# Kernel optimization log

Measured on AMD Instinct MI355X. Metric: run time of the kernel, lower is better.

Reference implementation:

```python
import jax, jax.numpy as jnp
import numpy as np

ATTEN_DIM = 64

def setup_inputs() -> dict:
    key = jax.random.key(0)
    ks = jax.random.split(key, 7)
    b, c, h, w = 16, 2048, 32, 32
    d_att, d_emb = 64, 64
    x = jax.random.normal(ks[0], (b, c, h, w), dtype=jnp.float32)
    # 1x1 conv == per-position linear; store weights as [out, in]
    scale = 1.0 / np.sqrt(c)
    wq = jax.random.normal(ks[1], (d_att, c), dtype=jnp.float32) * scale
    wk = jax.random.normal(ks[2], (d_att, c), dtype=jnp.float32) * scale
    wv = jax.random.normal(ks[3], (d_emb, c), dtype=jnp.float32) * scale
    bq = jnp.zeros((d_att,), dtype=jnp.float32)
    bk = jnp.zeros((d_att,), dtype=jnp.float32)
    bv = jnp.zeros((d_emb,), dtype=jnp.float32)
    return {"x": x, "wq": wq, "bq": bq, "wk": wk, "bk": bk, "wv": wv, "bv": bv}


def reference(x, wq, bq, wk, bk, wv, bv):
    b, c, h, w = x.shape
    # 1x1 conv projections: [b,c,h,w] x [d,c] -> [b,d,h,w]
    q = jnp.einsum('bchw,dc->bdhw', x, wq) + bq[None, :, None, None]
    k = jnp.einsum('bchw,dc->bdhw', x, wk) + bk[None, :, None, None]
    v = jnp.einsum('bchw,dc->bdhw', x, wv) + bv[None, :, None, None]
    # full non-local attention scores [b, h, w, h, w]
    atten = jnp.einsum('bcxy,bcij->bxyij', q, k) / ATTEN_DIM  # NOTE: module divides by atten_dim, not sqrt
    atten = jax.nn.softmax(atten.reshape(b, h, w, h * w), axis=-1).reshape(b, h, w, h, w)
    out = jnp.einsum('bxyij,bdij->bxyd', atten, v)
    return jnp.transpose(out, (0, 3, 1, 2))  # [b, emb_dim, h, w]
```

## Files before the change

kernel.cpp:

```cpp
#include <hip/hip_runtime.h>

typedef float f32x4 __attribute__((ext_vector_type(4)));
typedef short s16x8 __attribute__((ext_vector_type(8)));
typedef unsigned short u16;
typedef unsigned short u16x8 __attribute__((ext_vector_type(8)));

__device__ __forceinline__ u16 f2bf(float f) {
  unsigned u = __builtin_bit_cast(unsigned, f);
  u += 0x7fffu + ((u >> 16) & 1u);
  return (u16)(u >> 16);
}

__device__ __forceinline__ unsigned cvt_pk_bf16(float a, float b) {
  unsigned r;
  asm("v_cvt_pk_bf16_f32 %0, %1, %2" : "=v"(r) : "v"(a), "v"(b));
  return r;
}

#define AS1 __attribute__((address_space(1)))
#define AS3 __attribute__((address_space(3)))
#define GLD16(g, l) __builtin_amdgcn_global_load_lds((const AS1 unsigned int*)(g), (AS3 unsigned int*)(l), 16, 0, 0)

#define CEXP 0.0225421101f

__global__ __launch_bounds__(256) void prepack_w(
    const float* __restrict__ wq, const float* __restrict__ wk, const float* __restrict__ wv,
    u16* __restrict__ Wpk)
{
  const int d = blockIdx.x;
  const int t = threadIdx.x;
  const int kc = t >> 3, blk = t & 7;
  const int key = (d >> 1) & 7;
  const float* src = (d < 64) ? (wq + (size_t)d * 2048)
                   : (d < 128) ? (wk + (size_t)(d - 64) * 2048)
                               : (wv + (size_t)(d - 128) * 2048);
  const float* s8 = src + kc * 64 + ((blk ^ key) << 3);
  u16x8 o;
#pragma unroll
  for (int j = 0; j < 8; ++j) o[j] = f2bf(s8[j]);
  *(u16x8*)(Wpk + ((size_t)(kc * 192 + d) << 6) + (blk << 3)) = o;
}

__global__ __launch_bounds__(512) void qkv_proj(
    const float* __restrict__ x, const u16* __restrict__ Wpk,
    const float* __restrict__ bq, const float* __restrict__ bk, const float* __restrict__ bv,
    u16* __restrict__ Qo, u16* __restrict__ Ko, u16* __restrict__ Vt)
{
  const int b   = blockIdx.x >> 4;
  const int p0  = (blockIdx.x & 15) * 64;
  const int tid = threadIdx.x;
  const int lane = tid & 63;
  const int wid  = tid >> 6;
  const int l15 = lane & 15, l4 = lane >> 4;
  const int wm = wid & 1, wn = wid >> 1;

  __shared__ __align__(16) u16 lA[4][64 * 64];
  __shared__ __align__(16) u16 lB[4][192 * 64];

  const int pg = lane & 15;
  const int kb = wid * 4 + (lane >> 4);
  const int k0 = kb * 4;
  const int ww = wid - 4;

  f32x4 acc[2][3];
#pragma unroll
  for (int m = 0; m < 2; ++m)
#pragma unroll
    for (int n = 0; n < 3; ++n) acc[m][n] = (f32x4)(0.0f);

  const float* xb = x + (size_t)b * 2048 * 1024 + p0 + pg * 4;
  float4 SA[8], SB[8];

  auto xload2 = [&](int c, float4 (&S)[8]) {
#pragma unroll
    for (int cc = 0; cc < 2; ++cc) {
      const float* g = xb + (size_t)((c + cc) * 64 + k0) * 1024;
#pragma unroll
      for (int r = 0; r < 4; ++r) S[cc * 4 + r] = *(const float4*)(g + r * 1024);
    }
  };
  auto xstore2 = [&](int c, float4 (&S)[8]) {
#pragma unroll
    for (int cc = 0; cc < 2; ++cc) {
      const int slot = (c + cc) & 3;
#pragma unroll
      for (int col = 0; col < 4; ++col) {
        int p = pg * 4 + col;
        unsigned lo = cvt_pk_bf16(S[cc * 4 + 0][col], S[cc * 4 + 1][col]);
        unsigned hi = cvt_pk_bf16(S[cc * 4 + 2][col], S[cc * 4 + 3][col]);
        int swz = ((kb >> 1) ^ ((p >> 1) & 7)) & 7;
        char* dst = (char*)&lA[0][0] + slot * 8192 + p * 128 + (swz << 4) + (kb & 1) * 8;
        *(uint2*)dst = make_uint2(lo, hi);
      }
    }
  };
  auto wissue2 = [&](int c) {
#pragma unroll
    for (int cc = 0; cc < 2; ++cc) {
      const int slot = (c + cc) & 3;
      const u16* g = Wpk + (size_t)(c + cc) * 12288 + lane * 8;
#pragma unroll
      for (int j = 0; j < 6; ++j) {
        int q = ww * 6 + j;
        GLD16(g + q * 512, &lB[0][0] + slot * 12288 + q * 512);
      }
    }
  };
  auto domfma = [&](int slot) {
#pragma unroll
    for (int ks = 0; ks < 2; ++ks) {
      s16x8 af[2], bfv[3];
#pragma unroll
      for (int m = 0; m < 2; ++m) {
        int p = wm * 32 + m * 16 + l15;
        int swz = ((ks * 4 + l4) ^ ((p >> 1) & 7)) & 7;
        af[m] = *(const s16x8*)((const char*)&lA[0][0] + slot * 8192 + p * 128 + (swz << 4));
      }
#pragma unroll
      for (int n = 0; n < 3; ++n) {
        int d = wn * 48 + n * 16 + l15;
        int swz = ((ks * 4 + l4) ^ ((d >> 1) & 7)) & 7;
        bfv[n] = *(const s16x8*)((const char*)&lB[0][0] + slot * 24576 + d * 128 + (swz << 4));
      }
#pragma unroll
      for (int m = 0; m < 2; ++m)
#pragma unroll
        for (int n = 0; n < 3; ++n)
          acc[m][n] = __builtin_amdgcn_mfma_f32_16x16x32_bf16(af[m], bfv[n], acc[m][n], 0, 0, 0);
    }
  };
  auto barrier = [&]() {
    if (wid < 4) asm volatile("s_waitcnt lgkmcnt(0)" ::: "memory");
    else         asm volatile("s_waitcnt vmcnt(0) lgkmcnt(0)" ::: "memory");
    __builtin_amdgcn_sched_barrier(0);
    __builtin_amdgcn_s_barrier();
    __builtin_amdgcn_sched_barrier(0);
  };
  auto step = [&](int t, float4 (&Sl)[8], float4 (&Ss)[8]) {
    if (wid < 4) { if (t < 14) xload2(2 * t + 4, Sl); }
    else         { if (t < 15) wissue2(2 * t + 2); }
    __builtin_amdgcn_s_setprio(1);
    domfma((2 * t) & 3);
    domfma((2 * t + 1) & 3);
    __builtin_amdgcn_s_setprio(0);
    if (wid < 4 && t < 15) xstore2(2 * t + 2, Ss);
    barrier();
  };

  if (wid < 4) { xload2(0, SA); xload2(2, SB); xstore2(0, SA); }
  else         { wissue2(0); }
  barrier();

  for (int tt = 0; tt < 8; ++tt) {
    step(2 * tt,     SA, SB);
    step(2 * tt + 1, SB, SA);
  }

#pragma unroll
  for (int n = 0; n < 3; ++n) {
    const int dg = wn * 48 + n * 16 + l15;
    const int wi = dg >> 6, dl = dg & 63;
    const float* bsrc = (wi == 0) ? bq : (wi == 1) ? bk : bv;
    const float bias = bsrc[dl];
#pragma unroll
    for (int m = 0; m < 2; ++m) {
      const int pl = wm * 32 + m * 16 + l4 * 4;
      f32x4 a = acc[m][n];
      if (wi == 0) {
        u16* dst = Qo + ((size_t)b * 1024 + p0 + pl) * 64 + dl;
#pragma unroll
        for (int r = 0; r < 4; ++r) dst[(size_t)r * 64] = f2bf((a[r] + bias) * CEXP);
      } else if (wi == 1) {
#pragma unroll
        for (int r = 0; r < 4; ++r) {
          const int p = p0 + pl + r;
          Ko[((size_t)b * 1024 + p) * 64 + (((dl >> 3) ^ ((p >> 1) & 7)) << 3) + (dl & 7)]
            = f2bf(a[r] + bias);
        }
      } else {
        const int pk0 = p0 + pl;
        ushort4 hh;
        hh.x = f2bf(a[0] + bias); hh.y = f2bf(a[1] + bias);
        hh.z = f2bf(a[2] + bias); hh.w = f2bf(a[3] + bias);
        u16* dst = Vt + ((size_t)b * 64 + dl) * 1024 + (pk0 & ~127)
                 + (((((pk0 >> 3) & 15) ^ ((dl & 7) << 1)) & 15) << 3) + (pk0 & 7);
        *(ushort4*)dst = hh;
      }
    }
  }
}

__global__ __launch_bounds__(256) void attn_kernel(
    const u16* __restrict__ Qg, const u16* __restrict__ Kg,
    const u16* __restrict__ Vg, float* __restrict__ Po, float* __restrict__ lp)
{
  const int bid = blockIdx.x;
  const int b  = bid >> 5;
  const int qt = (bid >> 1) & 15;
  const int h  = bid & 1;
  const int q0 = qt * 64;
  const int tid = threadIdx.x;
  const int lane = tid & 63;
  const int w = tid >> 6;
  const int l15 = lane & 15, l4 = lane >> 4;
  const int qb = q0 + w * 16;

  __shared__ __align__(16) u16 lK[2][128 * 64];
  __shared__ __align__(16) u16 lV[2][64 * 128];
  __shared__ __align__(16) u16 lP[4][16 * 128];

  s16x8 qa[2];
#pragma unroll
  for (int ks = 0; ks < 2; ++ks)
    qa[ks] = *(const s16x8*)(Qg + ((size_t)b * 1024 + qb + l15) * 64 + ks * 32 + l4 * 8);

  const u16* Kb = Kg + (size_t)b * 65536;
  const u16* Vb = Vg + (size_t)b * 65536;

  float l_run[4];
  f32x4 oacc[4];
#pragma unroll
  for (int r = 0; r < 4; ++r) l_run[r] = 0.f;
#pragma unroll
  for (int n = 0; n < 4; ++n) oacc[n] = (f32x4)(0.0f);

  auto kv_issue = [&](int tile, int buf) {
    const int pk0 = tile * 128;
#pragma unroll
    for (int jj = 0; jj < 4; ++jj)
      GLD16(Kb + (size_t)(pk0 + w * 32 + jj * 8) * 64 + lane * 8,
            (char*)&lK[buf][0] + (w * 4 + jj) * 1024);
#pragma unroll
    for (int jj = 0; jj < 4; ++jj)
      GLD16(Vb + (size_t)(w * 16 + jj * 4 + (lane >> 4)) * 1024 + pk0 + (lane & 15) * 8,
            (char*)&lV[buf][0] + (w * 4 + jj) * 1024);
  };

  auto compute = [&](int buf) {
    f32x4 sacc[8];
#pragma unroll
    for (int n = 0; n < 8; ++n) sacc[n] = (f32x4)(0.0f);
    __builtin_amdgcn_s_setprio(1);
#pragma unroll
    for (int ks = 0; ks < 2; ++ks) {
#pragma unroll
      for (int n = 0; n < 8; ++n) {
        int row = n * 16 + l15;
        s16x8 kv = *(const s16x8*)(&lK[buf][0] + row * 64 +
                     (((ks * 4 + l4) ^ ((row >> 1) & 7)) << 3));
        sacc[n] = __builtin_amdgcn_mfma_f32_16x16x32_bf16(qa[ks], kv, sacc[n], 0, 0, 0);
      }
    }
    __builtin_amdgcn_s_setprio(0);

#pragma unroll
    for (int r = 0; r < 4; ++r) {
      const int prow = l4 * 4 + r;
      const int key = (prow & 7) << 1;
      float pv[8];
      float psum = 0.f;
#pragma unroll
      for (int n = 0; n < 8; ++n) { pv[n] = exp2f(sacc[n][r]); psum += pv[n]; }
#pragma unroll
      for (int n = 0; n < 8; n += 2) {
        unsigned pk = cvt_pk_bf16(pv[n], pv[n + 1]);
        int blk0 = (n * 2 + (l15 >> 3)) ^ key;
        int blk1 = ((n + 1) * 2 + (l15 >> 3)) ^ key;
        lP[w][prow * 128 + blk0 * 8 + (l15 & 7)] = (u16)pk;
        lP[w][prow * 128 + blk1 * 8 + (l15 & 7)] = (u16)(pk >> 16);
      }
      psum += __shfl_xor(psum, 1);
      psum += __shfl_xor(psum, 2);
      psum += __shfl_xor(psum, 4);
      psum += __shfl_xor(psum, 8);
      l_run[r] += psum;
    }

    __builtin_amdgcn_s_setprio(1);
#pragma unroll
    for (int ks = 0; ks < 4; ++ks) {
      s16x8 pfr = *(const s16x8*)(&lP[w][0] + l15 * 128 +
                    (((ks * 4 + l4) ^ ((l15 & 7) << 1)) << 3));
#pragma unroll
      for (int n = 0; n < 4; ++n) {
        int row = n * 16 + l15;
        s16x8 vv = *(const s16x8*)(&lV[buf][0] + row * 128 +
                     (((ks * 4 + l4) ^ ((row & 7) << 1)) << 3));
        oacc[n] = __builtin_amdgcn_mfma_f32_16x16x32_bf16(pfr, vv, oacc[n], 0, 0, 0);
      }
    }
    __builtin_amdgcn_s_setprio(0);
  };

  const int t0 = h * 4;
  kv_issue(t0, 0);
  kv_issue(t0 + 1, 1);
  asm volatile("s_waitcnt vmcnt(8)" ::: "memory");
  __builtin_amdgcn_sched_barrier(0);
  __builtin_amdgcn_s_barrier();
  __builtin_amdgcn_sched_barrier(0);

  for (int ic = 0; ic < 4; ++ic) {
    compute(ic & 1);
    if (ic < 3) {
      __builtin_amdgcn_sched_barrier(0);
      __builtin_amdgcn_s_barrier();
      __builtin_amdgcn_sched_barrier(0);
      if (ic + 2 < 4) {
        kv_issue(t0 + ic + 2, ic & 1);
        asm volatile("s_waitcnt vmcnt(8)" ::: "memory");
      } else {
        asm volatile("s_waitcnt vmcnt(0)" ::: "memory");
      }
      __builtin_amdgcn_sched_barrier(0);
      __builtin_amdgcn_s_barrier();
      __builtin_amdgcn_sched_barrier(0);
    }
  }

#pragma unroll
  for (int n = 0; n < 4; ++n) {
    const int d = n * 16 + l15;
    float4 o;
    o.x = oacc[n][0]; o.y = oacc[n][1]; o.z = oacc[n][2]; o.w = oacc[n][3];
    *(float4*)(Po + (((size_t)h * 16 + b) * 64 + d) * 1024 + q0 + w * 16 + l4 * 4) = o;
  }
  if (l15 == 0) {
#pragma unroll
    for (int r = 0; r < 4; ++r)
      lp[((size_t)h * 16 + b) * 1024 + qb + l4 * 4 + r] = l_run[r];
  }
}

__global__ __launch_bounds__(256) void attn_merge(
    const float* __restrict__ Po, const float* __restrict__ lp, float* __restrict__ out)
{
  const int i = (blockIdx.x * 256 + threadIdx.x) * 4;
  float4 a = *(const float4*)(Po + i);
  float4 c = *(const float4*)(Po + 1048576 + i);
  const int b = i >> 16;
  const int p = i & 1023;
  const float* l0 = lp + b * 1024 + p;
  const float* l1 = lp + 16384 + b * 1024 + p;
  float4 o;
  o.x = (a.x + c.x) / (l0[0] + l1[0]);
  o.y = (a.y + c.y) / (l0[1] + l1[1]);
  o.z = (a.z + c.z) / (l0[2] + l1[2]);
  o.w = (a.w + c.w) / (l0[3] + l1[3]);
  *(float4*)(out + i) = o;
}

extern "C" void kernel_launch(void* const* d_in, const int* in_sizes, int n_in,
                              void* d_out, int out_size, void* d_ws, size_t ws_size,
                              hipStream_t stream) {
  const float* x  = (const float*)d_in[0];
  const float* wq = (const float*)d_in[1];
  const float* bq = (const float*)d_in[2];
  const float* wk = (const float*)d_in[3];
  const float* bk = (const float*)d_in[4];
  const float* wv = (const float*)d_in[5];
  const float* bv = (const float*)d_in[6];
  float* out = (float*)d_out;

  u16* Qo  = (u16*)d_ws;
  u16* Ko  = Qo + (size_t)16 * 1024 * 64;
  u16* Vt  = Ko + (size_t)16 * 1024 * 64;
  u16* Wpk = Vt + (size_t)16 * 1024 * 64;
  float* Po = (float*)(Wpk + (size_t)32 * 192 * 64);
  float* lpart = Po + (size_t)2 * 16 * 64 * 1024;

  prepack_w<<<192, 256, 0, stream>>>(wq, wk, wv, Wpk);
  qkv_proj<<<256, 512, 0, stream>>>(x, Wpk, bq, bk, bv, Qo, Ko, Vt);
  attn_kernel<<<512, 256, 0, stream>>>(Qo, Ko, Vt, Po, lpart);
  attn_merge<<<1024, 256, 0, stream>>>(Po, lpart, out);
}
```

Before: 57.26 us.

## Fuse all four kernels into one cooperative persistent kernel with grid syncs

Replaces the prepack, QKV projection, attention and merge launches with one cooperative kernel of 256 blocks by 512 threads, separated by grid.sync barriers. The two key-halves of attention now run as two 256-thread halves of the same block and are merged through shared memory, which removes the global partial-output buffer and the separate merge pass. This is meant to cut launch gaps and global round-trips. In exchange it adds two grid-wide barriers and halves the attention grid to 256 blocks with a large 160KB shared allocation, so occupancy and parallelism drop.

```diff
diff --git a/kernel.cpp b/kernel.cpp
--- a/kernel.cpp
+++ b/kernel.cpp
@@ -1,4 +1,7 @@
 #include <hip/hip_runtime.h>
+#include <hip/hip_cooperative_groups.h>
+
+namespace cg = cooperative_groups;
 
 typedef float f32x4 __attribute__((ext_vector_type(4)));
 typedef short s16x8 __attribute__((ext_vector_type(8)));
@@ -23,331 +26,327 @@
 
 #define CEXP 0.0225421101f
 
-__global__ __launch_bounds__(256) void prepack_w(
-    const float* __restrict__ wq, const float* __restrict__ wk, const float* __restrict__ wv,
+__global__ __launch_bounds__(512) void fused_all(
+    const float* __restrict__ x,
+    const float* __restrict__ wq, const float* __restrict__ bq,
+    const float* __restrict__ wk, const float* __restrict__ bk,
+    const float* __restrict__ wv, const float* __restrict__ bv,
+    float* __restrict__ out,
+    u16* __restrict__ Qo, u16* __restrict__ Ko, u16* __restrict__ Vt,
     u16* __restrict__ Wpk)
 {
-  const int d = blockIdx.x;
-  const int t = threadIdx.x;
-  const int kc = t >> 3, blk = t & 7;
-  const int key = (d >> 1) & 7;
-  const float* src = (d < 64) ? (wq + (size_t)d * 2048)
-                   : (d < 128) ? (wk + (size_t)(d - 64) * 2048)
-                               : (wv + (size_t)(d - 128) * 2048);
-  const float* s8 = src + kc * 64 + ((blk ^ key) << 3);
-  u16x8 o;
-#pragma unroll
-  for (int j = 0; j < 8; ++j) o[j] = f2bf(s8[j]);
-  *(u16x8*)(Wpk + ((size_t)(kc * 192 + d) << 6) + (blk << 3)) = o;
-}
-
-__global__ __launch_bounds__(512) void qkv_proj(
-    const float* __restrict__ x, const u16* __restrict__ Wpk,
-    const float* __restrict__ bq, const float* __restrict__ bk, const float* __restrict__ bv,
-    u16* __restrict__ Qo, u16* __restrict__ Ko, u16* __restrict__ Vt)
-{
-  const int b   = blockIdx.x >> 4;
-  const int p0  = (blockIdx.x & 15) * 64;
+  cg::grid_group grid = cg::this_grid();
+  const int bid = blockIdx.x;
   const int tid = threadIdx.x;
   const int lane = tid & 63;
   const int wid  = tid >> 6;
   const int l15 = lane & 15, l4 = lane >> 4;
-  const int wm = wid & 1, wn = wid >> 1;
-
-  __shared__ __align__(16) u16 lA[4][64 * 64];
-  __shared__ __align__(16) u16 lB[4][192 * 64];
-
-  const int pg = lane & 15;
-  const int kb = wid * 4 + (lane >> 4);
-  const int k0 = kb * 4;
-  const int ww = wid - 4;
-
-  f32x4 acc[2][3];
-#pragma unroll
-  for (int m = 0; m < 2; ++m)
-#pragma unroll
-    for (int n = 0; n < 3; ++n) acc[m][n] = (f32x4)(0.0f);
-
-  const float* xb = x + (size_t)b * 2048 * 1024 + p0 + pg * 4;
-  float4 SA[8], SB[8];
-
-  auto xload2 = [&](int c, float4 (&S)[8]) {
-#pragma unroll
-    for (int cc = 0; cc < 2; ++cc) {
-      const float* g = xb + (size_t)((c + cc) * 64 + k0) * 1024;
-#pragma unroll
-      for (int r = 0; r < 4; ++r) S[cc * 4 + r] = *(const float4*)(g + r * 1024);
-    }
-  };
-  auto xstore2 = [&](int c, float4 (&S)[8]) {
-#pragma unroll
-    for (int cc = 0; cc < 2; ++cc) {
-      const int slot = (c + cc) & 3;
-#pragma unroll
-      for (int col = 0; col < 4; ++col) {
-        int p = pg * 4 + col;
-        unsigned lo = cvt_pk_bf16(S[cc * 4 + 0][col], S[cc * 4 + 1][col]);
-        unsigned hi = cvt_pk_bf16(S[cc * 4 + 2][col], S[cc * 4 + 3][col]);
-        int swz = ((kb >> 1) ^ ((p >> 1) & 7)) & 7;
-        char* dst = (char*)&lA[0][0] + slot * 8192 + p * 128 + (swz << 4) + (kb & 1) * 8;
-        *(uint2*)dst = make_uint2(lo, hi);
-      }
-    }
-  };
-  auto wissue2 = [&](int c) {
-#pragma unroll
-    for (int cc = 0; cc < 2; ++cc) {
-      const int slot = (c + cc) & 3;
-      const u16* g = Wpk + (size_t)(c + cc) * 12288 + lane * 8;
-#pragma unroll
-      for (int j = 0; j < 6; ++j) {
-        int q = ww * 6 + j;
-        GLD16(g + q * 512, &lB[0][0] + slot * 12288 + q * 512);
-      }
-    }
-  };
-  auto domfma = [&](int slot) {
-#pragma unroll
-    for (int ks = 0; ks < 2; ++ks) {
-      s16x8 af[2], bfv[3];
+  const int b  = bid >> 4;
+  const int p0 = (bid & 15) * 64;
+
+  __shared__ __align__(16) char smem[163840];
+
+  if (tid < 192) {
+    const int Gv = bid * 192 + tid;
+    const int kc = Gv / 1536;
+    const int r  = Gv % 1536;
+    const int d  = r >> 3;
+    const int blk = r & 7;
+    const int key = (d >> 1) & 7;
+    const float* src = (d < 64) ? (wq + (size_t)d * 2048)
+                     : (d < 128) ? (wk + (size_t)(d - 64) * 2048)
+                                 : (wv + (size_t)(d - 128) * 2048);
+    const float* s8 = src + kc * 64 + ((blk ^ key) << 3);
+    u16x8 o;
+#pragma unroll
+    for (int j = 0; j < 8; ++j) o[j] = f2bf(s8[j]);
+    *(u16x8*)(Wpk + ((size_t)(kc * 192 + d) << 6) + (blk << 3)) = o;
+  }
+  __threadfence();
+  grid.sync();
+
+  {
+    const int wm = wid & 1, wn = wid >> 1;
+    const int pg = lane & 15;
+    const int kb = wid * 4 + (lane >> 4);
+    const int k0 = kb * 4;
+    const int ww = wid - 4;
+
+    f32x4 acc[2][3];
+#pragma unroll
+    for (int m = 0; m < 2; ++m)
+#pragma unroll
+      for (int n = 0; n < 3; ++n) acc[m][n] = (f32x4)(0.0f);
+
+    const float* xb = x + (size_t)b * 2048 * 1024 + p0 + pg * 4;
+    float4 SA[8], SB[8];
+
+    auto xload2 = [&](int c, float4 (&S)[8]) {
+#pragma unroll
+      for (int cc = 0; cc < 2; ++cc) {
+        const float* g = xb + (size_t)((c + cc) * 64 + k0) * 1024;
+#pragma unroll
+        for (int r = 0; r < 4; ++r) S[cc * 4 + r] = *(const float4*)(g + r * 1024);
+      }
+    };
+    auto xstore2 = [&](int c, float4 (&S)[8]) {
+#pragma unroll
+      for (int cc = 0; cc < 2; ++cc) {
+        const int slot = (c + cc) & 3;
+#pragma unroll
+        for (int col = 0; col < 4; ++col) {
+          int p = pg * 4 + col;
+          unsigned lo = cvt_pk_bf16(S[cc * 4 + 0][col], S[cc * 4 + 1][col]);
+          unsigned hi = cvt_pk_bf16(S[cc * 4 + 2][col], S[cc * 4 + 3][col]);
+          int swz = ((kb >> 1) ^ ((p >> 1) & 7)) & 7;
+          *(uint2*)(smem + slot * 8192 + p * 128 + (swz << 4) + (kb & 1) * 8)
+            = make_uint2(lo, hi);
+        }
+      }
+    };
+    auto wissue2 = [&](int c) {
+#pragma unroll
+      for (int cc = 0; cc < 2; ++cc) {
+        const int slot = (c + cc) & 3;
+        const u16* g = Wpk + (size_t)(c + cc) * 12288 + lane * 8;
+#pragma unroll
+        for (int j = 0; j < 6; ++j) {
+          int q = ww * 6 + j;
+          GLD16(g + q * 512, smem + 32768 + slot * 24576 + q * 1024);
+        }
+      }
+    };
+    auto domfma = [&](int slot) {
+#pragma unroll
+      for (int ks = 0; ks < 2; ++ks) {
+        s16x8 af[2], bfv[3];
+#pragma unroll
+        for (int m = 0; m < 2; ++m) {
+          int p = wm * 32 + m * 16 + l15;
+          int swz = ((ks * 4 + l4) ^ ((p >> 1) & 7)) & 7;
+          af[m] = *(const s16x8*)(smem + slot * 8192 + p * 128 + (swz << 4));
+        }
+#pragma unroll
+        for (int n = 0; n < 3; ++n) {
+          int d = wn * 48 + n * 16 + l15;
+          int swz = ((ks * 4 + l4) ^ ((d >> 1) & 7)) & 7;
+          bfv[n] = *(const s16x8*)(smem + 32768 + slot * 24576 + d * 128 + (swz << 4));
+        }
+#pragma unroll
+        for (int m = 0; m < 2; ++m)
+#pragma unroll
+          for (int n = 0; n < 3; ++n)
+            acc[m][n] = __builtin_amdgcn_mfma_f32_16x16x32_bf16(af[m], bfv[n], acc[m][n], 0, 0, 0);
+      }
+    };
+    auto barrier = [&]() {
+      if (wid < 4) asm volatile("s_waitcnt lgkmcnt(0)" ::: "memory");
+      else         asm volatile("s_waitcnt vmcnt(0) lgkmcnt(0)" ::: "memory");
+      __builtin_amdgcn_sched_barrier(0);
+      __builtin_amdgcn_s_barrier();
+      __builtin_amdgcn_sched_barrier(0);
+    };
+    auto step = [&](int t, float4 (&Sl)[8], float4 (&Ss)[8]) {
+      if (wid < 4) { if (t < 14) xload2(2 * t + 4, Sl); }
+      else         { if (t < 15) wissue2(2 * t + 2); }
+      __builtin_amdgcn_s_setprio(1);
+      domfma((2 * t) & 3);
+      domfma((2 * t + 1) & 3);
+      __builtin_amdgcn_s_setprio(0);
+      if (wid < 4 && t < 15) xstore2(2 * t + 2, Ss);
+      barrier();
+    };
+
+    if (wid < 4) { xload2(0, SA); xload2(2, SB); xstore2(0, SA); }
+    else         { wissue2(0); }
+    barrier();
+
+    for (int tt = 0; tt < 8; ++tt) {
+      step(2 * tt,     SA, SB);
+      step(2 * tt + 1, SB, SA);
+    }
+
+#pragma unroll
+    for (int n = 0; n < 3; ++n) {
+      const int dg = wn * 48 + n * 16 + l15;
+      const int wi = dg >> 6, dl = dg & 63;
+      const float* bsrc = (wi == 0) ? bq : (wi == 1) ? bk : bv;
+      const float bias = bsrc[dl];
 #pragma unroll
       for (int m = 0; m < 2; ++m) {
-        int p = wm * 32 + m * 16 + l15;
-        int swz = ((ks * 4 + l4) ^ ((p >> 1) & 7)) & 7;
-        af[m] = *(const s16x8*)((const char*)&lA[0][0] + slot * 8192 + p * 128 + (swz << 4));
-      }
-#pragma unroll
-      for (int n = 0; n < 3; ++n) {
-        int d = wn * 48 + n * 16 + l15;
-        int swz = ((ks * 4 + l4) ^ ((d >> 1) & 7)) & 7;
-        bfv[n] = *(const s16x8*)((const char*)&lB[0][0] + slot * 24576 + d * 128 + (swz << 4));
-      }
-#pragma unroll
-      for (int m = 0; m < 2; ++m)
-#pragma unroll
-        for (int n = 0; n < 3; ++n)
-          acc[m][n] = __builtin_amdgcn_mfma_f32_16x16x32_bf16(af[m], bfv[n], acc[m][n], 0, 0, 0);
-    }
-  };
-  auto barrier = [&]() {
-    if (wid < 4) asm volatile("s_waitcnt lgkmcnt(0)" ::: "memory");
-    else         asm volatile("s_waitcnt vmcnt(0) lgkmcnt(0)" ::: "memory");
+        const int pl = wm * 32 + m * 16 + l4 * 4;
+        f32x4 a = acc[m][n];
+        if (wi == 0) {
+          u16* dst = Qo + ((size_t)b * 1024 + p0 + pl) * 64 + dl;
+#pragma unroll
+          for (int r = 0; r < 4; ++r) dst[(size_t)r * 64] = f2bf((a[r] + bias) * CEXP);
+        } else if (wi == 1) {
+#pragma unroll
+          for (int r = 0; r < 4; ++r) {
+            const int p = p0 + pl + r;
+            Ko[((size_t)b * 1024 + p) * 64 + (((dl >> 3) ^ ((p >> 1) & 7)) << 3) + (dl & 7)]
+              = f2bf(a[r] + bias);
+          }
+        } else {
+          const int pk0 = p0 + pl;
+          ushort4 hh;
+          hh.x = f2bf(a[0] + bias); hh.y = f2bf(a[1] + bias);
+          hh.z = f2bf(a[2] + bias); hh.w = f2bf(a[3] + bias);
+          u16* dst = Vt + ((size_t)b * 64 + dl) * 1024 + (pk0 & ~127)
+                   + (((((pk0 >> 3) & 15) ^ ((dl & 7) << 1)) & 15) << 3) + (pk0 & 7);
+          *(ushort4*)dst = hh;
+        }
+      }
+    }
+  }
+  __threadfence();
+  grid.sync();
+
+  {
+    const int h = wid >> 2;
+    const int w = wid & 3;
+    const int q0 = p0;
+    char* gbase = smem + h * 65536;
+    char* lPw   = smem + 131072 + wid * 4096;
+
+    s16x8 qa[2];
+#pragma unroll
+    for (int ks = 0; ks < 2; ++ks)
+      qa[ks] = *(const s16x8*)(Qo + ((size_t)b * 1024 + q0 + w * 16 + l15) * 64
+                               + ks * 32 + l4 * 8);
+
+    const u16* Kb = Ko + (size_t)b * 65536;
+    const u16* Vb = Vt + (size_t)b * 65536;
+
+    float l_run[4];
+    f32x4 oacc[4];
+#pragma unroll
+    for (int r = 0; r < 4; ++r) l_run[r] = 0.f;
+#pragma unroll
+    for (int n = 0; n < 4; ++n) oacc[n] = (f32x4)(0.0f);
+
+    auto kv_issue = [&](int tile, int buf) {
+      const int pk0 = tile * 128;
+#pragma unroll
+      for (int jj = 0; jj < 4; ++jj)
+        GLD16(Kb + (size_t)(pk0 + w * 32 + jj * 8) * 64 + lane * 8,
+              gbase + buf * 16384 + (w * 4 + jj) * 1024);
+#pragma unroll
+      for (int jj = 0; jj < 4; ++jj)
+        GLD16(Vb + (size_t)(w * 16 + jj * 4 + (lane >> 4)) * 1024 + pk0 + (lane & 15) * 8,
+              gbase + 32768 + buf * 16384 + (w * 4 + jj) * 1024);
+    };
+
+    auto compute = [&](int buf) {
+      const char* kB = gbase + buf * 16384;
+      const char* vB = gbase + 32768 + buf * 16384;
+      f32x4 sacc[8];
+#pragma unroll
+      for (int n = 0; n < 8; ++n) sacc[n] = (f32x4)(0.0f);
+      __builtin_amdgcn_s_setprio(1);
+#pragma unroll
+      for (int ks = 0; ks < 2; ++ks) {
+#pragma unroll
+        for (int n = 0; n < 8; ++n) {
+          int row = n * 16 + l15;
+          s16x8 kv = *(const s16x8*)(kB + row * 128 +
+                       ((((ks * 4 + l4) ^ ((row >> 1) & 7)) & 7) << 4));
+          sacc[n] = __builtin_amdgcn_mfma_f32_16x16x32_bf16(qa[ks], kv, sacc[n], 0, 0, 0);
+        }
+      }
+      __builtin_amdgcn_s_setprio(0);
+
+#pragma unroll
+      for (int r = 0; r < 4; ++r) {
+        const int prow = l4 * 4 + r;
+        const int key = (prow & 7) << 1;
+        float pv[8];
+        float psum = 0.f;
+#pragma unroll
+        for (int n = 0; n < 8; ++n) { pv[n] = exp2f(sacc[n][r]); psum += pv[n]; }
+#pragma unroll
+        for (int n = 0; n < 8; n += 2) {
+          unsigned pk = cvt_pk_bf16(pv[n], pv[n + 1]);
+          int blk0 = ((n * 2 + (l15 >> 3)) ^ key) & 15;
+          int blk1 = (((n + 1) * 2 + (l15 >> 3)) ^ key) & 15;
+          *(u16*)(lPw + prow * 256 + blk0 * 16 + (l15 & 7) * 2) = (u16)pk;
+          *(u16*)(lPw + prow * 256 + blk1 * 16 + (l15 & 7) * 2) = (u16)(pk >> 16);
+        }
+        psum += __shfl_xor(psum, 1);
+        psum += __shfl_xor(psum, 2);
+        psum += __shfl_xor(psum, 4);
+        psum += __shfl_xor(psum, 8);
+        l_run[r] += psum;
+      }
+
+      __builtin_amdgcn_s_setprio(1);
+#pragma unroll
+      for (int ks = 0; ks < 4; ++ks) {
+        s16x8 pfr = *(const s16x8*)(lPw + l15 * 256 +
+                      ((((ks * 4 + l4) ^ ((l15 & 7) << 1)) & 15) << 4));
+#pragma unroll
+        for (int n = 0; n < 4; ++n) {
+          int row = n * 16 + l15;
+          s16x8 vv = *(const s16x8*)(vB + row * 256 +
+                       ((((ks * 4 + l4) ^ ((row & 7) << 1)) & 15) << 4));
+          oacc[n] = __builtin_amdgcn_mfma_f32_16x16x32_bf16(pfr, vv, oacc[n], 0, 0, 0);
+        }
+      }
+      __builtin_amdgcn_s_setprio(0);
+    };
+
+    const int t0 = h * 4;
+    kv_issue(t0, 0);
+    kv_issue(t0 + 1, 1);
+    asm volatile("s_waitcnt vmcnt(8)" ::: "memory");
     __builtin_amdgcn_sched_barrier(0);
     __builtin_amdgcn_s_barrier();
     __builtin_amdgcn_sched_barrier(0);
-  };
-  auto step = [&](int t, float4 (&Sl)[8], float4 (&Ss)[8]) {
-    if (wid < 4) { if (t < 14) xload2(2 * t + 4, Sl); }
-    else         { if (t < 15) wissue2(2 * t + 2); }
-    __builtin_amdgcn_s_setprio(1);
-    domfma((2 * t) & 3);
-    domfma((2 * t + 1) & 3);
-    __builtin_amdgcn_s_setprio(0);
-    if (wid < 4 && t < 15) xstore2(2 * t + 2, Ss);
-    barrier();
-  };
-
-  if (wid < 4) { xload2(0, SA); xload2(2, SB); xstore2(0, SA); }
-  else         { wissue2(0); }
-  barrier();
-
-  for (int tt = 0; tt < 8; ++tt) {
-    step(2 * tt,     SA, SB);
-    step(2 * tt + 1, SB, SA);
+
+    for (int ic = 0; ic < 4; ++ic) {
+      compute(ic & 1);
+      if (ic < 3) {
+        __builtin_amdgcn_sched_barrier(0);
+        __builtin_amdgcn_s_barrier();
+        __builtin_amdgcn_sched_barrier(0);
+        if (ic + 2 < 4) {
+          kv_issue(t0 + ic + 2, ic & 1);
+          asm volatile("s_waitcnt vmcnt(8)" ::: "memory");
+        } else {
+          asm volatile("s_waitcnt vmcnt(0)" ::: "memory");
+        }
+        __builtin_amdgcn_sched_barrier(0);
+        __builtin_amdgcn_s_barrier();
+        __builtin_amdgcn_sched_barrier(0);
+      }
+    }
+
+    __syncthreads();
+    if (h == 1) {
+      float* mrg = (float*)smem + (tid - 256) * 20;
+#pragma unroll
+      for (int n = 0; n < 4; ++n) *(f32x4*)(mrg + n * 4) = oacc[n];
+#pragma unroll
+      for (int r = 0; r < 4; ++r) mrg[16 + r] = l_run[r];
+    }
+    __syncthreads();
+    if (h == 0) {
+      const float* mrg = (const float*)smem + tid * 20;
+      float lr[4];
+#pragma unroll
+      for (int r = 0; r < 4; ++r) lr[r] = l_run[r] + mrg[16 + r];
+#pragma unroll
+      for (int n = 0; n < 4; ++n) {
+        f32x4 o1 = *(const f32x4*)(mrg + n * 4);
+        float4 o;
+        o.x = (oacc[n][0] + o1[0]) / lr[0];
+        o.y = (oacc[n][1] + o1[1]) / lr[1];
+        o.z = (oacc[n][2] + o1[2]) / lr[2];
+        o.w = (oacc[n][3] + o1[3]) / lr[3];
+        *(float4*)(out + ((size_t)b * 64 + n * 16 + l15) * 1024 + q0 + w * 16 + l4 * 4) = o;
+      }
+    }
   }
-
-#pragma unroll
-  for (int n = 0; n < 3; ++n) {
-    const int dg = wn * 48 + n * 16 + l15;
-    const int wi = dg >> 6, dl = dg & 63;
-    const float* bsrc = (wi == 0) ? bq : (wi == 1) ? bk : bv;
-    const float bias = bsrc[dl];
-#pragma unroll
-    for (int m = 0; m < 2; ++m) {
-      const int pl = wm * 32 + m * 16 + l4 * 4;
-      f32x4 a = acc[m][n];
-      if (wi == 0) {
-        u16* dst = Qo + ((size_t)b * 1024 + p0 + pl) * 64 + dl;
-#pragma unroll
-        for (int r = 0; r < 4; ++r) dst[(size_t)r * 64] = f2bf((a[r] + bias) * CEXP);
-      } else if (wi == 1) {
-#pragma unroll
-        for (int r = 0; r < 4; ++r) {
-          const int p = p0 + pl + r;
-          Ko[((size_t)b * 1024 + p) * 64 + (((dl >> 3) ^ ((p >> 1) & 7)) << 3) + (dl & 7)]
-            = f2bf(a[r] + bias);
-        }
-      } else {
-        const int pk0 = p0 + pl;
-        ushort4 hh;
-        hh.x = f2bf(a[0] + bias); hh.y = f2bf(a[1] + bias);
-        hh.z = f2bf(a[2] + bias); hh.w = f2bf(a[3] + bias);
-        u16* dst = Vt + ((size_t)b * 64 + dl) * 1024 + (pk0 & ~127)
-                 + (((((pk0 >> 3) & 15) ^ ((dl & 7) << 1)) & 15) << 3) + (pk0 & 7);
-        *(ushort4*)dst = hh;
-      }
-    }
-  }
-}
-
-__global__ __launch_bounds__(256) void attn_kernel(
-    const u16* __restrict__ Qg, const u16* __restrict__ Kg,
-    const u16* __restrict__ Vg, float* __restrict__ Po, float* __restrict__ lp)
-{
-  const int bid = blockIdx.x;
-  const int b  = bid >> 5;
-  const int qt = (bid >> 1) & 15;
-  const int h  = bid & 1;
-  const int q0 = qt * 64;
-  const int tid = threadIdx.x;
-  const int lane = tid & 63;
-  const int w = tid >> 6;
-  const int l15 = lane & 15, l4 = lane >> 4;
-  const int qb = q0 + w * 16;
-
-  __shared__ __align__(16) u16 lK[2][128 * 64];
-  __shared__ __align__(16) u16 lV[2][64 * 128];
-  __shared__ __align__(16) u16 lP[4][16 * 128];
-
-  s16x8 qa[2];
-#pragma unroll
-  for (int ks = 0; ks < 2; ++ks)
-    qa[ks] = *(const s16x8*)(Qg + ((size_t)b * 1024 + qb + l15) * 64 + ks * 32 + l4 * 8);
-
-  const u16* Kb = Kg + (size_t)b * 65536;
-  const u16* Vb = Vg + (size_t)b * 65536;
-
-  float l_run[4];
-  f32x4 oacc[4];
-#pragma unroll
-  for (int r = 0; r < 4; ++r) l_run[r] = 0.f;
-#pragma unroll
-  for (int n = 0; n < 4; ++n) oacc[n] = (f32x4)(0.0f);
-
-  auto kv_issue = [&](int tile, int buf) {
-    const int pk0 = tile * 128;
-#pragma unroll
-    for (int jj = 0; jj < 4; ++jj)
-      GLD16(Kb + (size_t)(pk0 + w * 32 + jj * 8) * 64 + lane * 8,
-            (char*)&lK[buf][0] + (w * 4 + jj) * 1024);
-#pragma unroll
-    for (int jj = 0; jj < 4; ++jj)
-      GLD16(Vb + (size_t)(w * 16 + jj * 4 + (lane >> 4)) * 1024 + pk0 + (lane & 15) * 8,
-            (char*)&lV[buf][0] + (w * 4 + jj) * 1024);
-  };
-
-  auto compute = [&](int buf) {
-    f32x4 sacc[8];
-#pragma unroll
-    for (int n = 0; n < 8; ++n) sacc[n] = (f32x4)(0.0f);
-    __builtin_amdgcn_s_setprio(1);
-#pragma unroll
-    for (int ks = 0; ks < 2; ++ks) {
-#pragma unroll
-      for (int n = 0; n < 8; ++n) {
-        int row = n * 16 + l15;
-        s16x8 kv = *(const s16x8*)(&lK[buf][0] + row * 64 +
-                     (((ks * 4 + l4) ^ ((row >> 1) & 7)) << 3));
-        sacc[n] = __builtin_amdgcn_mfma_f32_16x16x32_bf16(qa[ks], kv, sacc[n], 0, 0, 0);
-      }
-    }
-    __builtin_amdgcn_s_setprio(0);
-
-#pragma unroll
-    for (int r = 0; r < 4; ++r) {
-      const int prow = l4 * 4 + r;
-      const int key = (prow & 7) << 1;
-      float pv[8];
-      float psum = 0.f;
-#pragma unroll
-      for (int n = 0; n < 8; ++n) { pv[n] = exp2f(sacc[n][r]); psum += pv[n]; }
-#pragma unroll
-      for (int n = 0; n < 8; n += 2) {
-        unsigned pk = cvt_pk_bf16(pv[n], pv[n + 1]);
-        int blk0 = (n * 2 + (l15 >> 3)) ^ key;
-        int blk1 = ((n + 1) * 2 + (l15 >> 3)) ^ key;
-        lP[w][prow * 128 + blk0 * 8 + (l15 & 7)] = (u16)pk;
-        lP[w][prow * 128 + blk1 * 8 + (l15 & 7)] = (u16)(pk >> 16);
-      }
-      psum += __shfl_xor(psum, 1);
-      psum += __shfl_xor(psum, 2);
-      psum += __shfl_xor(psum, 4);
-      psum += __shfl_xor(psum, 8);
-      l_run[r] += psum;
-    }
-
-    __builtin_amdgcn_s_setprio(1);
-#pragma unroll
-    for (int ks = 0; ks < 4; ++ks) {
-      s16x8 pfr = *(const s16x8*)(&lP[w][0] + l15 * 128 +
-                    (((ks * 4 + l4) ^ ((l15 & 7) << 1)) << 3));
-#pragma unroll
-      for (int n = 0; n < 4; ++n) {
-        int row = n * 16 + l15;
-        s16x8 vv = *(const s16x8*)(&lV[buf][0] + row * 128 +
-                     (((ks * 4 + l4) ^ ((row & 7) << 1)) << 3));
-        oacc[n] = __builtin_amdgcn_mfma_f32_16x16x32_bf16(pfr, vv, oacc[n], 0, 0, 0);
-      }
-    }
-    __builtin_amdgcn_s_setprio(0);
-  };
-
-  const int t0 = h * 4;
-  kv_issue(t0, 0);
-  kv_issue(t0 + 1, 1);
-  asm volatile("s_waitcnt vmcnt(8)" ::: "memory");
-  __builtin_amdgcn_sched_barrier(0);
-  __builtin_amdgcn_s_barrier();
-  __builtin_amdgcn_sched_barrier(0);
-
-  for (int ic = 0; ic < 4; ++ic) {
-    compute(ic & 1);
-    if (ic < 3) {
-      __builtin_amdgcn_sched_barrier(0);
-      __builtin_amdgcn_s_barrier();
-      __builtin_amdgcn_sched_barrier(0);
-      if (ic + 2 < 4) {
-        kv_issue(t0 + ic + 2, ic & 1);
-        asm volatile("s_waitcnt vmcnt(8)" ::: "memory");
-      } else {
-        asm volatile("s_waitcnt vmcnt(0)" ::: "memory");
-      }
-      __builtin_amdgcn_sched_barrier(0);
-      __builtin_amdgcn_s_barrier();
-      __builtin_amdgcn_sched_barrier(0);
-    }
-  }
-
-#pragma unroll
-  for (int n = 0; n < 4; ++n) {
-    const int d = n * 16 + l15;
-    float4 o;
-    o.x = oacc[n][0]; o.y = oacc[n][1]; o.z = oacc[n][2]; o.w = oacc[n][3];
-    *(float4*)(Po + (((size_t)h * 16 + b) * 64 + d) * 1024 + q0 + w * 16 + l4 * 4) = o;
-  }
-  if (l15 == 0) {
-#pragma unroll
-    for (int r = 0; r < 4; ++r)
-      lp[((size_t)h * 16 + b) * 1024 + qb + l4 * 4 + r] = l_run[r];
-  }
-}
-
-__global__ __launch_bounds__(256) void attn_merge(
-    const float* __restrict__ Po, const float* __restrict__ lp, float* __restrict__ out)
-{
-  const int i = (blockIdx.x * 256 + threadIdx.x) * 4;
-  float4 a = *(const float4*)(Po + i);
-  float4 c = *(const float4*)(Po + 1048576 + i);
-  const int b = i >> 16;
-  const int p = i & 1023;
-  const float* l0 = lp + b * 1024 + p;
-  const float* l1 = lp + 16384 + b * 1024 + p;
-  float4 o;
-  o.x = (a.x + c.x) / (l0[0] + l1[0]);
-  o.y = (a.y + c.y) / (l0[1] + l1[1]);
-  o.z = (a.z + c.z) / (l0[2] + l1[2]);
-  o.w = (a.w + c.w) / (l0[3] + l1[3]);
-  *(float4*)(out + i) = o;
 }
 
 extern "C" void kernel_launch(void* const* d_in, const int* in_sizes, int n_in,
@@ -366,11 +365,9 @@
   u16* Ko  = Qo + (size_t)16 * 1024 * 64;
   u16* Vt  = Ko + (size_t)16 * 1024 * 64;
   u16* Wpk = Vt + (size_t)16 * 1024 * 64;
-  float* Po = (float*)(Wpk + (size_t)32 * 192 * 64);
-  float* lpart = Po + (size_t)2 * 16 * 64 * 1024;
-
-  prepack_w<<<192, 256, 0, stream>>>(wq, wk, wv, Wpk);
-  qkv_proj<<<256, 512, 0, stream>>>(x, Wpk, bq, bk, bv, Qo, Ko, Vt);
-  attn_kernel<<<512, 256, 0, stream>>>(Qo, Ko, Vt, Po, lpart);
-  attn_merge<<<1024, 256, 0, stream>>>(Po, lpart, out);
+
+  void* args[] = { (void*)&x, (void*)&wq, (void*)&bq, (void*)&wk, (void*)&bk,
+                   (void*)&wv, (void*)&bv, (void*)&out,
+                   (void*)&Qo, (void*)&Ko, (void*)&Vt, (void*)&Wpk };
+  hipLaunchCooperativeKernel((void*)fused_all, dim3(256), dim3(512), args, 0, stream);
 }
```

Measured after the change: 226.6 us. 296% more time.

## Split attention KV range four ways instead of two across blocks

Applied to the files above, without the earlier changes.

Each batch/query tile is now split into four KV chunks of 256 keys (two tiles each) instead of two chunks of 512, launching 1024 attention blocks rather than 512. The merge kernel sums four partial outputs and four partial normalizers. The aim is more parallelism and better CU occupancy on a 256-CU-class GPU. The cost is twice the partial-output traffic, a heavier merge, and a shorter per-block pipeline with less load/compute overlap. It relies on the softmax partials sharing a fixed exponent offset, as the existing two-way split already did.

```diff
diff --git a/kernel.cpp b/kernel.cpp
--- a/kernel.cpp
+++ b/kernel.cpp
@@ -195,9 +195,9 @@
     const u16* __restrict__ Vg, float* __restrict__ Po, float* __restrict__ lp)
 {
   const int bid = blockIdx.x;
-  const int b  = bid >> 5;
-  const int qt = (bid >> 1) & 15;
-  const int h  = bid & 1;
+  const int b  = bid >> 6;
+  const int qt = (bid >> 2) & 15;
+  const int qr = bid & 3;
   const int q0 = qt * 64;
   const int tid = threadIdx.x;
   const int lane = tid & 63;
@@ -292,7 +292,7 @@
     __builtin_amdgcn_s_setprio(0);
   };
 
-  const int t0 = h * 4;
+  const int t0 = qr * 2;
   kv_issue(t0, 0);
   kv_issue(t0 + 1, 1);
   asm volatile("s_waitcnt vmcnt(8)" ::: "memory");
@@ -300,35 +300,27 @@
   __builtin_amdgcn_s_barrier();
   __builtin_amdgcn_sched_barrier(0);
 
-  for (int ic = 0; ic < 4; ++ic) {
-    compute(ic & 1);
-    if (ic < 3) {
-      __builtin_amdgcn_sched_barrier(0);
-      __builtin_amdgcn_s_barrier();
-      __builtin_amdgcn_sched_barrier(0);
-      if (ic + 2 < 4) {
-        kv_issue(t0 + ic + 2, ic & 1);
-        asm volatile("s_waitcnt vmcnt(8)" ::: "memory");
-      } else {
-        asm volatile("s_waitcnt vmcnt(0)" ::: "memory");
-      }
-      __builtin_amdgcn_sched_barrier(0);
-      __builtin_amdgcn_s_barrier();
-      __builtin_amdgcn_sched_barrier(0);
-    }
-  }
+  compute(0);
+  __builtin_amdgcn_sched_barrier(0);
+  __builtin_amdgcn_s_barrier();
+  __builtin_amdgcn_sched_barrier(0);
+  asm volatile("s_waitcnt vmcnt(0)" ::: "memory");
+  __builtin_amdgcn_sched_barrier(0);
+  __builtin_amdgcn_s_barrier();
+  __builtin_amdgcn_sched_barrier(0);
+  compute(1);
 
 #pragma unroll
   for (int n = 0; n < 4; ++n) {
     const int d = n * 16 + l15;
     float4 o;
     o.x = oacc[n][0]; o.y = oacc[n][1]; o.z = oacc[n][2]; o.w = oacc[n][3];
-    *(float4*)(Po + (((size_t)h * 16 + b) * 64 + d) * 1024 + q0 + w * 16 + l4 * 4) = o;
+    *(float4*)(Po + (((size_t)qr * 16 + b) * 64 + d) * 1024 + q0 + w * 16 + l4 * 4) = o;
   }
   if (l15 == 0) {
 #pragma unroll
     for (int r = 0; r < 4; ++r)
-      lp[((size_t)h * 16 + b) * 1024 + qb + l4 * 4 + r] = l_run[r];
+      lp[((size_t)qr * 16 + b) * 1024 + qb + l4 * 4 + r] = l_run[r];
   }
 }
 
@@ -336,17 +328,20 @@
     const float* __restrict__ Po, const float* __restrict__ lp, float* __restrict__ out)
 {
   const int i = (blockIdx.x * 256 + threadIdx.x) * 4;
-  float4 a = *(const float4*)(Po + i);
-  float4 c = *(const float4*)(Po + 1048576 + i);
   const int b = i >> 16;
   const int p = i & 1023;
-  const float* l0 = lp + b * 1024 + p;
-  const float* l1 = lp + 16384 + b * 1024 + p;
+  float4 s = *(const float4*)(Po + i);
+  float l0 = lp[b * 1024 + p + 0], l1 = lp[b * 1024 + p + 1];
+  float l2 = lp[b * 1024 + p + 2], l3 = lp[b * 1024 + p + 3];
+#pragma unroll
+  for (int q = 1; q < 4; ++q) {
+    float4 c = *(const float4*)(Po + (size_t)q * 1048576 + i);
+    s.x += c.x; s.y += c.y; s.z += c.z; s.w += c.w;
+    const float* lq = lp + (size_t)q * 16384 + b * 1024 + p;
+    l0 += lq[0]; l1 += lq[1]; l2 += lq[2]; l3 += lq[3];
+  }
   float4 o;
-  o.x = (a.x + c.x) / (l0[0] + l1[0]);
-  o.y = (a.y + c.y) / (l0[1] + l1[1]);
-  o.z = (a.z + c.z) / (l0[2] + l1[2]);
-  o.w = (a.w + c.w) / (l0[3] + l1[3]);
+  o.x = s.x / l0; o.y = s.y / l1; o.z = s.z / l2; o.w = s.w / l3;
   *(float4*)(out + i) = o;
 }
 
@@ -367,10 +362,10 @@
   u16* Vt  = Ko + (size_t)16 * 1024 * 64;
   u16* Wpk = Vt + (size_t)16 * 1024 * 64;
   float* Po = (float*)(Wpk + (size_t)32 * 192 * 64);
-  float* lpart = Po + (size_t)2 * 16 * 64 * 1024;
+  float* lpart = Po + (size_t)4 * 16 * 64 * 1024;
 
   prepack_w<<<192, 256, 0, stream>>>(wq, wk, wv, Wpk);
   qkv_proj<<<256, 512, 0, stream>>>(x, Wpk, bq, bk, bv, Qo, Ko, Vt);
-  attn_kernel<<<512, 256, 0, stream>>>(Qo, Ko, Vt, Po, lpart);
+  attn_kernel<<<1024, 256, 0, stream>>>(Qo, Ko, Vt, Po, lpart);
   attn_merge<<<1024, 256, 0, stream>>>(Po, lpart, out);
 }
```

Result: slower. 60.30 us (+5.3%).

## Keep softmax P in registers by transposing QK MFMA and permuting K rows

Applied to the files above, without the earlier changes.

Swaps the MFMA operand order so the score tile comes out transposed (keys along rows, queries along lanes). Each lane's exp values can then be packed directly into the A-operand fragment for the PV MFMA, with no LDS round trip. To make the key ordering match the fragment layout, the projection kernel writes K rows in a permuted position order. This removes the lP shared buffer, its stores and loads, and the per-row shuffle reductions. The cost is a coupled layout change between the two kernels and a final shuffle to recover per-row sums.

```diff
diff --git a/kernel.cpp b/kernel.cpp
--- a/kernel.cpp
+++ b/kernel.cpp
@@ -2,6 +2,7 @@
 
 typedef float f32x4 __attribute__((ext_vector_type(4)));
 typedef short s16x8 __attribute__((ext_vector_type(8)));
+typedef unsigned u32x4 __attribute__((ext_vector_type(4)));
 typedef unsigned short u16;
 typedef unsigned short u16x8 __attribute__((ext_vector_type(8)));
 
@@ -174,7 +175,8 @@
 #pragma unroll
         for (int r = 0; r < 4; ++r) {
           const int p = p0 + pl + r;
-          Ko[((size_t)b * 1024 + p) * 64 + (((dl >> 3) ^ ((p >> 1) & 7)) << 3) + (dl & 7)]
+          const int p2 = (p & ~28) | ((p & 8) >> 1) | ((p & 16) >> 1) | ((p & 4) << 2);
+          Ko[((size_t)b * 1024 + p2) * 64 + (((dl >> 3) ^ ((p2 >> 1) & 7)) << 3) + (dl & 7)]
             = f2bf(a[r] + bias);
         }
       } else {
@@ -207,7 +209,6 @@
 
   __shared__ __align__(16) u16 lK[2][128 * 64];
   __shared__ __align__(16) u16 lV[2][64 * 128];
-  __shared__ __align__(16) u16 lP[4][16 * 128];
 
   s16x8 qa[2];
 #pragma unroll
@@ -217,10 +218,8 @@
   const u16* Kb = Kg + (size_t)b * 65536;
   const u16* Vb = Vg + (size_t)b * 65536;
 
-  float l_run[4];
+  float l_run = 0.f;
   f32x4 oacc[4];
-#pragma unroll
-  for (int r = 0; r < 4; ++r) l_run[r] = 0.f;
 #pragma unroll
   for (int n = 0; n < 4; ++n) oacc[n] = (f32x4)(0.0f);
 
@@ -248,39 +247,36 @@
         int row = n * 16 + l15;
         s16x8 kv = *(const s16x8*)(&lK[buf][0] + row * 64 +
                      (((ks * 4 + l4) ^ ((row >> 1) & 7)) << 3));
-        sacc[n] = __builtin_amdgcn_mfma_f32_16x16x32_bf16(qa[ks], kv, sacc[n], 0, 0, 0);
+        sacc[n] = __builtin_amdgcn_mfma_f32_16x16x32_bf16(kv, qa[ks], sacc[n], 0, 0, 0);
       }
     }
     __builtin_amdgcn_s_setprio(0);
 
-#pragma unroll
-    for (int r = 0; r < 4; ++r) {
-      const int prow = l4 * 4 + r;
-      const int key = (prow & 7) << 1;
-      float pv[8];
-      float psum = 0.f;
-#pragma unroll
-      for (int n = 0; n < 8; ++n) { pv[n] = exp2f(sacc[n][r]); psum += pv[n]; }
-#pragma unroll
-      for (int n = 0; n < 8; n += 2) {
-        unsigned pk = cvt_pk_bf16(pv[n], pv[n + 1]);
-        int blk0 = (n * 2 + (l15 >> 3)) ^ key;
-        int blk1 = ((n + 1) * 2 + (l15 >> 3)) ^ key;
-        lP[w][prow * 128 + blk0 * 8 + (l15 & 7)] = (u16)pk;
-        lP[w][prow * 128 + blk1 * 8 + (l15 & 7)] = (u16)(pk >> 16);
-      }
-      psum += __shfl_xor(psum, 1);
-      psum += __shfl_xor(psum, 2);
-      psum += __shfl_xor(psum, 4);
-      psum += __shfl_xor(psum, 8);
-      l_run[r] += psum;
-    }
+    unsigned c[8][2];
+    float psum = 0.f;
+#pragma unroll
+    for (int n = 0; n < 8; ++n) {
+      float e0 = exp2f(sacc[n][0]);
+      float e1 = exp2f(sacc[n][1]);
+      float e2 = exp2f(sacc[n][2]);
+      float e3 = exp2f(sacc[n][3]);
+      psum += (e0 + e1) + (e2 + e3);
+      c[n][0] = cvt_pk_bf16(e0, e1);
+      c[n][1] = cvt_pk_bf16(e2, e3);
+    }
+    psum += __shfl_xor(psum, 16);
+    psum += __shfl_xor(psum, 32);
+    l_run += psum;
 
     __builtin_amdgcn_s_setprio(1);
 #pragma unroll
     for (int ks = 0; ks < 4; ++ks) {
-      s16x8 pfr = *(const s16x8*)(&lP[w][0] + l15 * 128 +
-                    (((ks * 4 + l4) ^ ((l15 & 7) << 1)) << 3));
+      u32x4 t;
+      t[0] = c[2 * ks][0];
+      t[1] = c[2 * ks][1];
+      t[2] = c[2 * ks + 1][0];
+      t[3] = c[2 * ks + 1][1];
+      s16x8 pfr = __builtin_bit_cast(s16x8, t);
 #pragma unroll
       for (int n = 0; n < 4; ++n) {
         int row = n * 16 + l15;
@@ -318,6 +314,10 @@
     }
   }
 
+  float lr[4];
+#pragma unroll
+  for (int r = 0; r < 4; ++r) lr[r] = __shfl(l_run, l4 * 4 + r);
+
 #pragma unroll
   for (int n = 0; n < 4; ++n) {
     const int d = n * 16 + l15;
@@ -328,7 +328,7 @@
   if (l15 == 0) {
 #pragma unroll
     for (int r = 0; r < 4; ++r)
-      lp[((size_t)h * 16 + b) * 1024 + qb + l4 * 4 + r] = l_run[r];
+      lp[((size_t)h * 16 + b) * 1024 + qb + l4 * 4 + r] = lr[r];
   }
 }
 
```

Result: faster. 55.40 us (-3.3%).
